# Kernel optimization log

Hardware: AMD Instinct MI355X
Metric: run time of the kernel (lower is better)

The kernel has to match this reference:

```python
import jax, jax.numpy as jnp
import numpy as np

B, T, K = 512, 512, 128
START, STOP = K - 2, K - 1
NEG = -10000.0


def setup_inputs() -> dict:
    key = jax.random.key(0)
    k1, k2, k3 = jax.random.split(key, 3)
    feats = jax.random.normal(k1, (B, T, K), dtype=jnp.float32)
    # gold tags exclude START/STOP
    tags = jax.random.randint(k2, (B, T), 0, K - 2)
    transitions = jax.random.normal(k3, (K, K), dtype=jnp.float32)
    # __init__ pins: transitions[START, :] = -10000 ; transitions[:, STOP] = -10000
    transitions = transitions.at[START, :].set(NEG).at[:, STOP].set(NEG)
    return {"feats": feats, "tags": tags, "transitions": transitions}


def _forward_alg(feats, transitions):
    # feats: [B, T, K]; CRF partition function via log-space semiring scan
    Bb, Tt, Kk = feats.shape
    alpha0 = jnp.full((Bb, Kk), NEG, dtype=feats.dtype).at[:, START].set(0.0)

    def step(alpha, feat):  # alpha: [B, K_prev], feat: [B, K_next]
        # score[b, next, prev] = alpha[b, prev] + T[next, prev] + feat[b, next]
        s = alpha[:, None, :] + transitions[None, :, :] + feat[:, :, None]
        return jax.nn.logsumexp(s, axis=-1), None

    alpha, _ = jax.lax.scan(step, alpha0, jnp.swapaxes(feats, 0, 1))
    return jax.nn.logsumexp(alpha + transitions[STOP], axis=-1)  # [B]


def _score_sentence(feats, tags, transitions):
    # score of the gold path, fully vectorized over time
    Bb = feats.shape[0]
    start = jnp.full((Bb, 1), START, dtype=tags.dtype)
    ext = jnp.concatenate([start, tags], axis=1)  # [B, T+1]
    trans_score = transitions[ext[:, 1:], ext[:, :-1]].sum(axis=1)  # [B]
    emit_score = jnp.take_along_axis(feats, tags[:, :, None], axis=2)[..., 0].sum(axis=1)
    return trans_score + emit_score + transitions[STOP, ext[:, -1]]


def reference(feats, tags, transitions):
    # neg_log_likelihood: mean over batch of (log Z - gold path score)
    forward_score = _forward_alg(feats, transitions)
    gold_score = _score_sentence(feats, tags, transitions)
    return jnp.sum(forward_score - gold_score) / feats.shape[0]
```

## Files before the change

### kernel.cpp

```cpp
#include <hip/hip_runtime.h>
#include <math.h>

#define Bb 512
#define Tt 512
#define Kk 128
#define NSTART 126
#define NSTOP  127

static constexpr float LOG2E = 1.4426950408889634f;
static constexpr float LN2   = 0.6931471805599453f;

__device__ __forceinline__ float fexp2(float x){ return __builtin_amdgcn_exp2f(x); }
__device__ __forceinline__ float flog2(float x){ return __builtin_amdgcn_logf(x); }
__device__ __forceinline__ float frcp (float x){ return __builtin_amdgcn_rcpf(x); }

__device__ __forceinline__ void dot2a(float& acc, unsigned int e, int s){
  asm("v_dot2_f32_f16 %0, %1, %2, %0" : "+v"(acc) : "v"(e), "s"(s));
}
__device__ __forceinline__ unsigned int pk2f16(float lo, float hi){
  unsigned int u; asm("v_cvt_pkrtz_f16_f32 %0, %1, %2" : "=v"(u) : "v"(lo), "v"(hi)); return u;
}
__device__ __forceinline__ float cvt_f32_f16(unsigned int u){
  float f; asm("v_cvt_f32_f16 %0, %1" : "=v"(f) : "v"(u)); return f;
}

template<int CTRL>
__device__ __forceinline__ float dpp_mov(float s){
  union {float f; int i;} a, r; a.f = s;
  r.i = __builtin_amdgcn_update_dpp(a.i, a.i, CTRL, 0xf, 0xf, false);
  return r.f;
}
#define QP_XOR1  0xB1
#define QP_XOR2  0x4E
#define ROW_ROR4 0x124
#define ROW_ROR8 0x128

__device__ __forceinline__ float rlanef(float x, int lane){
  union {float f; int i;} v; v.f = x;
  union {int i; float f;} r; r.i = __builtin_amdgcn_readlane(v.i, lane);
  return r.f;
}

__global__ __launch_bounds__(64, 1) void crf_rl(
    const float* __restrict__ feats,
    const int*   __restrict__ tags,
    const float* __restrict__ trans,
    float* __restrict__ part)
{
  const int b = blockIdx.x;
  const int l = threadIdx.x;

  unsigned int E0[64], E1[64];
  {
    const float* t0 = trans + (size_t)(2*l)     * Kk;
    const float* t1 = trans + (size_t)(2*l + 1) * Kk;
    #pragma unroll
    for (int j = 0; j < 64; ++j) {
      float2 v0 = *(const float2*)(t0 + 2*j);
      float2 v1 = *(const float2*)(t1 + 2*j);
      E0[j] = pk2f16(fexp2(v0.x * LOG2E), fexp2(v0.y * LOG2E));
      E1[j] = pk2f16(fexp2(v1.x * LOG2E), fexp2(v1.y * LOG2E));
    }
  }
  #pragma unroll
  for (int j = 0; j < 64; ++j)
    asm volatile("" : "+v"(E0[j]), "+v"(E1[j]));

  unsigned int a = (l == 63) ? 0x00003C00u : 0u;

  const float* fp2 = feats + (size_t)b * Tt * Kk + 2*l;
  float2 F[4];
  #pragma unroll
  for (int i = 0; i < 4; ++i) F[i] = *(const float2*)(fp2 + (size_t)i * Kk);

  float C2 = 0.0f;

  for (int t = 0; t < Tt; t += 4) {
    #pragma unroll
    for (int u = 0; u < 4; ++u) {
      const float f0 = F[u].x, f1 = F[u].y;
      {
        int tn = t + 4 + u; if (tn > Tt - 1) tn = Tt - 1;
        F[u] = *(const float2*)(fp2 + (size_t)tn * Kk);
      }

      float A0=0.f,A1=0.f,A2=0.f,A3=0.f, B0=0.f,B1=0.f,B2=0.f,B3=0.f;
      #pragma unroll
      for (int i = 0; i < 64; i += 4) {
        const int s0 = __builtin_amdgcn_readlane((int)a, i+0);
        const int s1 = __builtin_amdgcn_readlane((int)a, i+1);
        const int s2 = __builtin_amdgcn_readlane((int)a, i+2);
        const int s3 = __builtin_amdgcn_readlane((int)a, i+3);
        dot2a(A0, E0[i+0], s0);  dot2a(B0, E1[i+0], s0);
        dot2a(A1, E0[i+1], s1);  dot2a(B1, E1[i+1], s1);
        dot2a(A2, E0[i+2], s2);  dot2a(B2, E1[i+2], s2);
        dot2a(A3, E0[i+3], s3);  dot2a(B3, E1[i+3], s3);
      }
      const float sA = (A0 + A1) + (A2 + A3);
      const float sB = (B0 + B1) + (B2 + B3);
      float y0 = fexp2(f0 * LOG2E) * sA;
      float y1 = fexp2(f1 * LOG2E) * sB;

      float m = fmaxf(y0, y1);
      m = fmaxf(m, dpp_mov<QP_XOR1>(m));
      m = fmaxf(m, dpp_mov<QP_XOR2>(m));
      m = fmaxf(m, dpp_mov<ROW_ROR4>(m));
      m = fmaxf(m, dpp_mov<ROW_ROR8>(m));
      const float mm = fmaxf(fmaxf(rlanef(m, 0),  rlanef(m, 16)),
                             fmaxf(rlanef(m, 32), rlanef(m, 48)));
      C2 += flog2(mm);
      const float inv = frcp(mm);
      a = pk2f16(y0 * inv, y1 * inv);
    }
  }

  {
    const float a0 = cvt_f32_f16(a);
    const float a1 = cvt_f32_f16(a >> 16);
    const float e0 = fexp2(trans[(size_t)NSTOP * Kk + 2*l]     * LOG2E);
    const float e1 = fexp2(trans[(size_t)NSTOP * Kk + 2*l + 1] * LOG2E);
    float v = a0 * e0 + a1 * e1;
    #pragma unroll
    for (int off = 32; off >= 1; off >>= 1) v += __shfl_xor(v, off, 64);
    const float fwd = LN2 * (C2 + flog2(v));

    const int* tg = tags + (size_t)b * Tt;
    const float* fbase = feats + (size_t)b * Tt * Kk;
    float g = 0.0f;
    #pragma unroll
    for (int k2 = 0; k2 < Tt / 64; ++k2) {
      const int tt   = l + 64 * k2;
      const int curt = tg[tt];
      const int prv  = (tt == 0) ? NSTART : tg[tt - 1];
      g += trans[(size_t)curt * Kk + prv] + fbase[(size_t)tt * Kk + curt];
    }
    if (l == 0) g += trans[(size_t)NSTOP * Kk + tg[Tt - 1]];
    #pragma unroll
    for (int off = 32; off >= 1; off >>= 1) g += __shfl_xor(g, off, 64);

    if (l == 0) part[b] = fwd - g;
  }
}

__global__ __launch_bounds__(256) void reduce_mean_kernel(
    const float* __restrict__ part, float* __restrict__ out)
{
  __shared__ float buf[4];
  const int tid = threadIdx.x;
  float v = part[tid] + part[tid + 256];
  #pragma unroll
  for (int off = 32; off >= 1; off >>= 1) v += __shfl_xor(v, off, 64);
  if ((tid & 63) == 0) buf[tid >> 6] = v;
  __syncthreads();
  if (tid == 0)
    out[0] = (buf[0] + buf[1] + buf[2] + buf[3]) * (1.0f / (float)Bb);
}

extern "C" void kernel_launch(void* const* d_in, const int* in_sizes, int n_in,
                              void* d_out, int out_size, void* d_ws, size_t ws_size,
                              hipStream_t stream) {
  const float* feats = (const float*)d_in[0];
  const int*   tags  = (const int*)d_in[1];
  const float* trans = (const float*)d_in[2];
  float* part = (float*)d_ws;

  crf_rl<<<dim3(Bb), dim3(64), 0, stream>>>(feats, tags, trans, part);
  reduce_mean_kernel<<<dim3(1), dim3(256), 0, stream>>>(part, (float*)d_out);
}
```

Baseline: 270.4 us.

## Batch 16 sequences per block and run CRF recurrence on MFMA

Replaces the one-wave-per-sequence dot2 recurrence with a 256-thread block that handles 16 sequences at once. Each step becomes a 128x128 by 128x16 fp16 matrix product on MFMA 16x16x32, with alpha exchanged through double-buffered LDS and a block barrier per step. Normalisation uses the previous step's max with a fixed offset, which keeps the scaling reduction off the critical path. The change raises arithmetic density but launches only 32 blocks, uses far fewer CUs, and adds a __syncthreads to every step of the serial chain.

```diff
diff --git a/kernel.cpp b/kernel.cpp
--- a/kernel.cpp
+++ b/kernel.cpp
@@ -1,144 +1,188 @@
 #include <hip/hip_runtime.h>
 #include <math.h>
+#include <stdint.h>
 
 #define Bb 512
 #define Tt 512
 #define Kk 128
 #define NSTART 126
 #define NSTOP  127
+#define G 16
+#define NBLK (Bb/G)
+#define NTHR 256
 
 static constexpr float LOG2E = 1.4426950408889634f;
 static constexpr float LN2   = 0.6931471805599453f;
 
+typedef _Float16 f16x8 __attribute__((ext_vector_type(8)));
+typedef float    f32x4 __attribute__((ext_vector_type(4)));
+
 __device__ __forceinline__ float fexp2(float x){ return __builtin_amdgcn_exp2f(x); }
 __device__ __forceinline__ float flog2(float x){ return __builtin_amdgcn_logf(x); }
-__device__ __forceinline__ float frcp (float x){ return __builtin_amdgcn_rcpf(x); }
-
-__device__ __forceinline__ void dot2a(float& acc, unsigned int e, int s){
-  asm("v_dot2_f32_f16 %0, %1, %2, %0" : "+v"(acc) : "v"(e), "s"(s));
-}
-__device__ __forceinline__ unsigned int pk2f16(float lo, float hi){
-  unsigned int u; asm("v_cvt_pkrtz_f16_f32 %0, %1, %2" : "=v"(u) : "v"(lo), "v"(hi)); return u;
-}
-__device__ __forceinline__ float cvt_f32_f16(unsigned int u){
-  float f; asm("v_cvt_f32_f16 %0, %1" : "=v"(f) : "v"(u)); return f;
-}
-
-template<int CTRL>
-__device__ __forceinline__ float dpp_mov(float s){
-  union {float f; int i;} a, r; a.f = s;
-  r.i = __builtin_amdgcn_update_dpp(a.i, a.i, CTRL, 0xf, 0xf, false);
-  return r.f;
-}
-#define QP_XOR1  0xB1
-#define QP_XOR2  0x4E
-#define ROW_ROR4 0x124
-#define ROW_ROR8 0x128
-
-__device__ __forceinline__ float rlanef(float x, int lane){
-  union {float f; int i;} v; v.f = x;
-  union {int i; float f;} r; r.i = __builtin_amdgcn_readlane(v.i, lane);
-  return r.f;
-}
-
-__global__ __launch_bounds__(64, 1) void crf_rl(
+
+__device__ __forceinline__ unsigned pkh(float lo, float hi){
+  union { _Float16 h[2]; unsigned u; } p;
+  p.h[0] = (_Float16)lo; p.h[1] = (_Float16)hi;
+  return p.u;
+}
+
+__global__ __launch_bounds__(NTHR) void crf_mfma(
     const float* __restrict__ feats,
     const int*   __restrict__ tags,
     const float* __restrict__ trans,
     float* __restrict__ part)
 {
-  const int b = blockIdx.x;
-  const int l = threadIdx.x;
-
-  unsigned int E0[64], E1[64];
+  const int tid = threadIdx.x;
+  const int w   = tid >> 6;
+  const int l   = tid & 63;
+  const int c   = l & 15;
+  const int g   = l >> 4;
+  const int B0  = blockIdx.x * G;
+
+  __shared__ __align__(16) unsigned bufU[2][4][64][4];
+  __shared__ float Mp[2][4][G];
+  __shared__ float fwdS[G];
+  __shared__ float gpart[G][17];
+
+  f16x8 E[2][4];
+  #pragma unroll
+  for (int mt2 = 0; mt2 < 2; ++mt2) {
+    const int mrow = 32*w + 16*mt2 + c;
+    #pragma unroll
+    for (int kt = 0; kt < 4; ++kt) {
+      const float* tr = trans + (size_t)mrow * Kk + kt*32 + g*8;
+      float4 v0 = *reinterpret_cast<const float4*>(tr);
+      float4 v1 = *reinterpret_cast<const float4*>(tr + 4);
+      E[mt2][kt][0] = (_Float16)fexp2(v0.x * LOG2E);
+      E[mt2][kt][1] = (_Float16)fexp2(v0.y * LOG2E);
+      E[mt2][kt][2] = (_Float16)fexp2(v0.z * LOG2E);
+      E[mt2][kt][3] = (_Float16)fexp2(v0.w * LOG2E);
+      E[mt2][kt][4] = (_Float16)fexp2(v1.x * LOG2E);
+      E[mt2][kt][5] = (_Float16)fexp2(v1.y * LOG2E);
+      E[mt2][kt][6] = (_Float16)fexp2(v1.z * LOG2E);
+      E[mt2][kt][7] = (_Float16)fexp2(v1.w * LOG2E);
+    }
+  }
+
+  #pragma unroll
+  for (int mt2 = 0; mt2 < 2; ++mt2) {
+    float y[4];
+    #pragma unroll
+    for (int reg = 0; reg < 4; ++reg)
+      y[reg] = (32*w + 16*mt2 + 4*g + reg == NSTART) ? 1.0f : 0.0f;
+    unsigned* dst = &bufU[0][w][c + 16*(2*mt2 + (g>>1))][2*(g&1)];
+    *reinterpret_cast<uint2*>(dst) = make_uint2(pkh(y[0], y[1]), pkh(y[2], y[3]));
+  }
+  if (l < G) Mp[0][w][l] = (w == 3) ? 1.0f : 0.0f;
+
+  const float* fb = feats + (size_t)(B0 + c) * Tt * Kk + 32*w + 4*g;
+  float4 F[2][2];
+  F[0][0] = *reinterpret_cast<const float4*>(fb);
+  F[0][1] = *reinterpret_cast<const float4*>(fb + 16);
+  F[1][0] = *reinterpret_cast<const float4*>(fb + Kk);
+  F[1][1] = *reinterpret_cast<const float4*>(fb + Kk + 16);
+
+  float C2 = 0.0f;
+  __syncthreads();
+
+  for (int t = 0; t < Tt; ++t) {
+    const int cur = t & 1, nxt = cur ^ 1;
+
+    f16x8 Bf[4];
+    #pragma unroll
+    for (int kt = 0; kt < 4; ++kt) {
+      union { uint4 u; f16x8 h; } cv;
+      cv.u = *reinterpret_cast<const uint4*>(&bufU[cur][kt][l][0]);
+      Bf[kt] = cv.h;
+    }
+    const float Mmax = fmaxf(fmaxf(Mp[cur][0][c], Mp[cur][1][c]),
+                             fmaxf(Mp[cur][2][c], Mp[cur][3][c]));
+    const float lm  = flog2(Mmax);
+    const float lsc = -6.0f - lm;
+    C2 += lm + 6.0f;
+
+    f32x4 acc0 = {0.f, 0.f, 0.f, 0.f}, acc1 = {0.f, 0.f, 0.f, 0.f};
+    #pragma unroll
+    for (int kt = 0; kt < 4; ++kt) {
+      acc0 = __builtin_amdgcn_mfma_f32_16x16x32_f16(E[0][kt], Bf[kt], acc0, 0, 0, 0);
+      acc1 = __builtin_amdgcn_mfma_f32_16x16x32_f16(E[1][kt], Bf[kt], acc1, 0, 0, 0);
+    }
+
+    const float4 f0 = F[cur][0], f1 = F[cur][1];
+    {
+      int tn = t + 2; if (tn > Tt - 1) tn = Tt - 1;
+      F[cur][0] = *reinterpret_cast<const float4*>(fb + (size_t)tn * Kk);
+      F[cur][1] = *reinterpret_cast<const float4*>(fb + (size_t)tn * Kk + 16);
+    }
+
+    float y0[4], y1[4];
+    const float fr0[4] = {f0.x, f0.y, f0.z, f0.w};
+    const float fr1[4] = {f1.x, f1.y, f1.z, f1.w};
+    #pragma unroll
+    for (int reg = 0; reg < 4; ++reg) {
+      y0[reg] = acc0[reg] * fexp2(fmaf(fr0[reg], LOG2E, lsc));
+      y1[reg] = acc1[reg] * fexp2(fmaf(fr1[reg], LOG2E, lsc));
+    }
+
+    float pm = fmaxf(fmaxf(fmaxf(y0[0], y0[1]), fmaxf(y0[2], y0[3])),
+                     fmaxf(fmaxf(y1[0], y1[1]), fmaxf(y1[2], y1[3])));
+    pm = fmaxf(pm, __shfl_xor(pm, 16, 64));
+    pm = fmaxf(pm, __shfl_xor(pm, 32, 64));
+    if (l < G) Mp[nxt][w][l] = pm;
+
+    #pragma unroll
+    for (int mt2 = 0; mt2 < 2; ++mt2) {
+      const float* y = (mt2 == 0) ? y0 : y1;
+      unsigned* dst = &bufU[nxt][w][c + 16*(2*mt2 + (g>>1))][2*(g&1)];
+      *reinterpret_cast<uint2*>(dst) = make_uint2(pkh(y[0], y[1]), pkh(y[2], y[3]));
+    }
+    __syncthreads();
+  }
+
   {
-    const float* t0 = trans + (size_t)(2*l)     * Kk;
-    const float* t1 = trans + (size_t)(2*l + 1) * Kk;
-    #pragma unroll
-    for (int j = 0; j < 64; ++j) {
-      float2 v0 = *(const float2*)(t0 + 2*j);
-      float2 v1 = *(const float2*)(t1 + 2*j);
-      E0[j] = pk2f16(fexp2(v0.x * LOG2E), fexp2(v0.y * LOG2E));
-      E1[j] = pk2f16(fexp2(v1.x * LOG2E), fexp2(v1.y * LOG2E));
-    }
-  }
-  #pragma unroll
-  for (int j = 0; j < 64; ++j)
-    asm volatile("" : "+v"(E0[j]), "+v"(E1[j]));
-
-  unsigned int a = (l == 63) ? 0x00003C00u : 0u;
-
-  const float* fp2 = feats + (size_t)b * Tt * Kk + 2*l;
-  float2 F[4];
-  #pragma unroll
-  for (int i = 0; i < 4; ++i) F[i] = *(const float2*)(fp2 + (size_t)i * Kk);
-
-  float C2 = 0.0f;
-
-  for (int t = 0; t < Tt; t += 4) {
-    #pragma unroll
-    for (int u = 0; u < 4; ++u) {
-      const float f0 = F[u].x, f1 = F[u].y;
-      {
-        int tn = t + 4 + u; if (tn > Tt - 1) tn = Tt - 1;
-        F[u] = *(const float2*)(fp2 + (size_t)tn * Kk);
-      }
-
-      float A0=0.f,A1=0.f,A2=0.f,A3=0.f, B0=0.f,B1=0.f,B2=0.f,B3=0.f;
+    float v = 0.0f;
+    #pragma unroll
+    for (int kt = 0; kt < 4; ++kt) {
+      union { uint4 u; f16x8 h; } cv;
+      cv.u = *reinterpret_cast<const uint4*>(&bufU[0][kt][l][0]);
+      const float* ts = trans + (size_t)NSTOP * Kk + kt*32 + g*8;
+      float4 s0 = *reinterpret_cast<const float4*>(ts);
+      float4 s1 = *reinterpret_cast<const float4*>(ts + 4);
+      const float sv[8] = {s0.x, s0.y, s0.z, s0.w, s1.x, s1.y, s1.z, s1.w};
       #pragma unroll
-      for (int i = 0; i < 64; i += 4) {
-        const int s0 = __builtin_amdgcn_readlane((int)a, i+0);
-        const int s1 = __builtin_amdgcn_readlane((int)a, i+1);
-        const int s2 = __builtin_amdgcn_readlane((int)a, i+2);
-        const int s3 = __builtin_amdgcn_readlane((int)a, i+3);
-        dot2a(A0, E0[i+0], s0);  dot2a(B0, E1[i+0], s0);
-        dot2a(A1, E0[i+1], s1);  dot2a(B1, E1[i+1], s1);
-        dot2a(A2, E0[i+2], s2);  dot2a(B2, E1[i+2], s2);
-        dot2a(A3, E0[i+3], s3);  dot2a(B3, E1[i+3], s3);
-      }
-      const float sA = (A0 + A1) + (A2 + A3);
-      const float sB = (B0 + B1) + (B2 + B3);
-      float y0 = fexp2(f0 * LOG2E) * sA;
-      float y1 = fexp2(f1 * LOG2E) * sB;
-
-      float m = fmaxf(y0, y1);
-      m = fmaxf(m, dpp_mov<QP_XOR1>(m));
-      m = fmaxf(m, dpp_mov<QP_XOR2>(m));
-      m = fmaxf(m, dpp_mov<ROW_ROR4>(m));
-      m = fmaxf(m, dpp_mov<ROW_ROR8>(m));
-      const float mm = fmaxf(fmaxf(rlanef(m, 0),  rlanef(m, 16)),
-                             fmaxf(rlanef(m, 32), rlanef(m, 48)));
-      C2 += flog2(mm);
-      const float inv = frcp(mm);
-      a = pk2f16(y0 * inv, y1 * inv);
-    }
-  }
+      for (int j = 0; j < 8; ++j)
+        v = fmaf((float)cv.h[j], fexp2(sv[j] * LOG2E), v);
+    }
+    v += __shfl_xor(v, 16, 64);
+    v += __shfl_xor(v, 32, 64);
+    const float fwd = LN2 * (C2 + flog2(v));
+    if (w == 0 && l < G) fwdS[l] = fwd;
+  }
+  __syncthreads();
 
   {
-    const float a0 = cvt_f32_f16(a);
-    const float a1 = cvt_f32_f16(a >> 16);
-    const float e0 = fexp2(trans[(size_t)NSTOP * Kk + 2*l]     * LOG2E);
-    const float e1 = fexp2(trans[(size_t)NSTOP * Kk + 2*l + 1] * LOG2E);
-    float v = a0 * e0 + a1 * e1;
-    #pragma unroll
-    for (int off = 32; off >= 1; off >>= 1) v += __shfl_xor(v, off, 64);
-    const float fwd = LN2 * (C2 + flog2(v));
-
-    const int* tg = tags + (size_t)b * Tt;
-    const float* fbase = feats + (size_t)b * Tt * Kk;
-    float g = 0.0f;
-    #pragma unroll
-    for (int k2 = 0; k2 < Tt / 64; ++k2) {
-      const int tt   = l + 64 * k2;
+    const int c2  = tid & 15;
+    const int seg = tid >> 4;
+    const int bc  = B0 + c2;
+    const int* tg = tags + (size_t)bc * Tt;
+    const float* fbase = feats + (size_t)bc * Tt * Kk;
+    const int t0 = seg * 32;
+    int prev = (t0 == 0) ? NSTART : tg[t0 - 1];
+    float gg = 0.0f;
+    for (int tt = t0; tt < t0 + 32; ++tt) {
       const int curt = tg[tt];
-      const int prv  = (tt == 0) ? NSTART : tg[tt - 1];
-      g += trans[(size_t)curt * Kk + prv] + fbase[(size_t)tt * Kk + curt];
-    }
-    if (l == 0) g += trans[(size_t)NSTOP * Kk + tg[Tt - 1]];
-    #pragma unroll
-    for (int off = 32; off >= 1; off >>= 1) g += __shfl_xor(g, off, 64);
-
-    if (l == 0) part[b] = fwd - g;
+      gg += trans[(size_t)curt * Kk + prev] + fbase[(size_t)tt * Kk + curt];
+      prev = curt;
+    }
+    if (seg == 15) gg += trans[(size_t)NSTOP * Kk + tg[Tt - 1]];
+    gpart[c2][seg] = gg;
+  }
+  __syncthreads();
+  if (tid < G) {
+    float gold = 0.0f;
+    #pragma unroll
+    for (int s = 0; s < 16; ++s) gold += gpart[tid][s];
+    part[B0 + tid] = fwdS[tid] - gold;
   }
 }
 
@@ -164,6 +208,6 @@
   const float* trans = (const float*)d_in[2];
   float* part = (float*)d_ws;
 
-  crf_rl<<<dim3(Bb), dim3(64), 0, stream>>>(feats, tags, trans, part);
+  crf_mfma<<<dim3(NBLK), dim3(NTHR), 0, stream>>>(feats, tags, trans, part);
   reduce_mean_kernel<<<dim3(1), dim3(256), 0, stream>>>(part, (float*)d_out);
 }
```

After: 551.3 us. +103.9%, slower.
